# Optimization experiments

Measured on AMD Instinct MI355X. Metric: run time of the kernel, lower is better.

The kernel has to match this reference:

```python
import jax, jax.numpy as jnp
import numpy as np

B, S, D, H, HD, KVH, FF = 2, 2048, 2048, 16, 128, 1, 8192
EPS = 1e-6
ROPE_BASE = 10000.0
NEG = -1e9


def _rms_norm(x, w):
    return x * jax.lax.rsqrt(jnp.mean(x * x, axis=-1, keepdims=True) + EPS) * w


def _rope(t):
    # t: [B, S, H, HD]; standard rotate-half RoPE
    half = HD // 2
    inv_freq = ROPE_BASE ** (-jnp.arange(0, HD, 2, dtype=jnp.float32) / HD)  # [half]
    ang = jnp.arange(S, dtype=jnp.float32)[:, None] * inv_freq               # [S, half]
    cos = jnp.concatenate([jnp.cos(ang), jnp.cos(ang)], axis=-1)[None, :, None, :]
    sin = jnp.concatenate([jnp.sin(ang), jnp.sin(ang)], axis=-1)[None, :, None, :]
    t1, t2 = t[..., :half], t[..., half:]
    rot = jnp.concatenate([-t2, t1], axis=-1)
    return t * cos + rot * sin


def _alibi_bias():
    # slopes for power-of-two head count: 2^(-8*(h+1)/H)
    slopes = 2.0 ** (-8.0 * (jnp.arange(H, dtype=jnp.float32) + 1.0) / H)    # [H]
    pos = jnp.arange(S, dtype=jnp.float32)
    dist = jnp.abs(pos[:, None] - pos[None, :])                              # [S, S]
    return (-slopes[:, None, None] * dist)[None]                             # [1, H, S, S]


def setup_inputs() -> dict:
    key = jax.random.key(0)
    ks = jax.random.split(key, 8)
    sc = lambda fan: 1.0 / np.sqrt(fan)
    x = jax.random.normal(ks[0], (B, S, D), jnp.float32)
    causal = jnp.where(jnp.tril(jnp.ones((S, S), bool)), 0.0, NEG).astype(jnp.float32)[None, None]
    return {
        "x": x,
        "mask": causal,                                                       # [1,1,S,S]
        "w_norm1": jnp.ones((D,), jnp.float32),
        "w_norm2": jnp.ones((D,), jnp.float32),
        "q_w": jax.random.normal(ks[1], (D, D), jnp.float32) * sc(D),        # [out,in] torch layout
        "kv_w": jax.random.normal(ks[2], (KVH * HD * 2, D), jnp.float32) * sc(D),
        "o_w": jax.random.normal(ks[3], (D, D), jnp.float32) * sc(D),
        "w1": jax.random.normal(ks[4], (FF, D), jnp.float32) * sc(D),
        "w2": jax.random.normal(ks[5], (FF, D), jnp.float32) * sc(D),
        "w3": jax.random.normal(ks[6], (D, FF), jnp.float32) * sc(FF),
    }


def reference(x, mask, w_norm1, w_norm2, q_w, kv_w, o_w, w1, w2, w3):
    # --- attention sub-block (pre-norm) ---
    h = _rms_norm(x, w_norm1)
    q = (h @ q_w.T).reshape(B, S, H, HD)                                      # [B,S,H,HD]
    kv = (h @ kv_w.T).reshape(B, S, KVH, 2, HD)
    k = jnp.broadcast_to(kv[:, :, :, 0, :], (B, S, H, HD))                    # MQA expand
    v = jnp.broadcast_to(kv[:, :, :, 1, :], (B, S, H, HD))
    q, k = _rope(q), _rope(k)
    scores = jnp.einsum('bshd,bthd->bhst', q, k) / np.sqrt(HD)                # [B,H,S,S]
    scores = scores + _alibi_bias() + mask
    attn = jax.nn.softmax(scores, axis=-1)
    out = jnp.einsum('bhst,bthd->bshd', attn, v).reshape(B, S, D)
    x = x + out @ o_w.T
    # --- SwiGLU FFN sub-block (pre-norm) ---
    h2 = _rms_norm(x, w_norm2)
    gated = jax.nn.silu(h2 @ w1.T) * (h2 @ w2.T)                              # [B,S,FF]
    return x + gated @ w3.T
```

## Files before the change

kernel.cpp:

```cpp
#include <hip/hip_runtime.h>
#include <stdint.h>

#define NB 2
#define NS 2048
#define ND 2048
#define NH 16
#define NHD 128
#define NFF 8192
#define NBS (NB*NS)
#define NQKV 2304

typedef unsigned short u16;
typedef __attribute__((ext_vector_type(8))) short bf16x8;
typedef __attribute__((ext_vector_type(4))) unsigned short u16x4;
typedef __attribute__((ext_vector_type(4))) float f32x4;

__device__ __forceinline__ u16 f2bf(float f) {
  union { float f; unsigned u; } v; v.f = f;
  unsigned r = v.u + 0x7fffu + ((v.u >> 16) & 1u);
  return (u16)(r >> 16);
}
__device__ __forceinline__ float bf2f(u16 h) {
  union { unsigned u; float f; } v; v.u = ((unsigned)h) << 16;
  return v.f;
}
__device__ __forceinline__ void async_cp16(const void* g, void* l) {
  __builtin_amdgcn_global_load_lds((const __attribute__((address_space(1))) void*)g,
                                   (__attribute__((address_space(3))) void*)l, 16, 0, 0);
}

__global__ void cvt_bf16_kernel(const float* __restrict__ in, u16* __restrict__ out, int n4) {
  int i = blockIdx.x * blockDim.x + threadIdx.x;
  if (i >= n4) return;
  float4 v = reinterpret_cast<const float4*>(in)[i];
  u16x4 o; o.x = f2bf(v.x); o.y = f2bf(v.y); o.z = f2bf(v.z); o.w = f2bf(v.w);
  reinterpret_cast<u16x4*>(out)[i] = o;
}

__global__ __launch_bounds__(256) void rmsnorm_kernel(const float* __restrict__ x,
                                                      const float* __restrict__ w,
                                                      u16* __restrict__ out) {
  const int row = blockIdx.x, tid = threadIdx.x;
  const float* xr = x + (size_t)row * ND;
  float4 a = *reinterpret_cast<const float4*>(xr + tid * 8);
  float4 b = *reinterpret_cast<const float4*>(xr + tid * 8 + 4);
  float ss = a.x*a.x + a.y*a.y + a.z*a.z + a.w*a.w
           + b.x*b.x + b.y*b.y + b.z*b.z + b.w*b.w;
#pragma unroll
  for (int off = 32; off > 0; off >>= 1) ss += __shfl_down(ss, off);
  __shared__ float red[4];
  __shared__ float rinv_s;
  if ((tid & 63) == 0) red[tid >> 6] = ss;
  __syncthreads();
  if (tid == 0) rinv_s = rsqrtf((red[0] + red[1] + red[2] + red[3]) * (1.0f / ND) + 1e-6f);
  __syncthreads();
  const float rinv = rinv_s;
  const float* wr = w + tid * 8;
  u16* orow = out + (size_t)row * ND + tid * 8;
  float vs[8] = {a.x, a.y, a.z, a.w, b.x, b.y, b.z, b.w};
#pragma unroll
  for (int j = 0; j < 8; ++j) orow[j] = f2bf(vs[j] * rinv * wr[j]);
}

__global__ void rope_table_kernel(float* __restrict__ cosT, float* __restrict__ sinT) {
  int i = blockIdx.x * blockDim.x + threadIdx.x;
  if (i >= NS * 64) return;
  int s = i >> 6, d = i & 63;
  float freq = expf(-(float)d * (9.210340371976184f / 64.0f));
  float ang = (float)s * freq;
  cosT[i] = cosf(ang);
  sinT[i] = sinf(ang);
}

__global__ void rope_q_kernel(const u16* __restrict__ qkvraw, const float* __restrict__ cosT,
                              const float* __restrict__ sinT, u16* __restrict__ qout) {
  int i = blockIdx.x * blockDim.x + threadIdx.x;
  if (i >= NB * NS * NH * 64) return;
  int d = i & 63, h = (i >> 6) & 15, s = (i >> 10) & (NS - 1), b = i >> 21;
  size_t rrow = ((size_t)(b * NS + s)) * NQKV + h * NHD;
  float t1 = bf2f(qkvraw[rrow + d]);
  float t2 = bf2f(qkvraw[rrow + d + 64]);
  float c = cosT[(s << 6) + d], sn = sinT[(s << 6) + d];
  const float scale = 0.08838834764831845f;
  size_t orow = (((size_t)(b * NH + h)) * NS + s) * NHD;
  qout[orow + d]      = f2bf((t1 * c - t2 * sn) * scale);
  qout[orow + d + 64] = f2bf((t2 * c + t1 * sn) * scale);
}

__global__ void rope_kv_kernel(const u16* __restrict__ qkvraw, const float* __restrict__ cosT,
                               const float* __restrict__ sinT, u16* __restrict__ kout,
                               u16* __restrict__ vtout) {
  int i = blockIdx.x * blockDim.x + threadIdx.x;
  if (i >= NB * NS * 64) return;
  int d = i & 63, s = (i >> 6) & (NS - 1), b = i >> 17;
  size_t rrow = ((size_t)(b * NS + s)) * NQKV + ND;
  float t1 = bf2f(qkvraw[rrow + d]);
  float t2 = bf2f(qkvraw[rrow + d + 64]);
  float c = cosT[(s << 6) + d], sn = sinT[(s << 6) + d];
  size_t orow = ((size_t)(b * NS + s)) * NHD;
  kout[orow + d]      = f2bf(t1 * c - t2 * sn);
  kout[orow + d + 64] = f2bf(t2 * c + t1 * sn);
  vtout[((size_t)(b * 128 + d)) * NS + s]      = qkvraw[rrow + 128 + d];
  vtout[((size_t)(b * 128 + d + 64)) * NS + s] = qkvraw[rrow + 128 + d + 64];
}

template <int EPI>
__global__ __launch_bounds__(256) void gemm3_kernel(const u16* __restrict__ A,
                                                    const u16* __restrict__ W,
                                                    void* Out, const void* Aux,
                                                    int M, int N, int K) {
  __shared__ __align__(16) char As[128 * 128];
  __shared__ __align__(16) char Bs[128 * 128];
  const int tid = threadIdx.x, wave = tid >> 6, lane = tid & 63;
  const int lm = lane & 15, lg = lane >> 4;

  int bx, by;
  {
    const int gx = gridDim.x;
    if ((gx & 7) == 0) {
      const int id = blockIdx.y * gx + blockIdx.x;
      const int xcd = id & 7, rank = id >> 3;
      const int cw = gx >> 3;
      bx = xcd * cw + rank % cw;
      by = rank / cw;
    } else { bx = blockIdx.x; by = blockIdx.y; }
  }
  const int m0 = by * 128, n0 = bx * 128;
  const int wr = wave >> 1, wc = wave & 1;

  f32x4 acc[4][4];
#pragma unroll
  for (int i = 0; i < 4; ++i)
#pragma unroll
    for (int j = 0; j < 4; ++j) acc[i][j] = (f32x4){0.f, 0.f, 0.f, 0.f};

  for (int k0 = 0; k0 < K; k0 += 64) {
#pragma unroll
    for (int p = 0; p < 4; ++p) {
      int X = p * 4096 + tid * 16;
      int r = X >> 7;
      int sw = ((X >> 4) ^ (X >> 7)) & 7;
      async_cp16(A + (size_t)(m0 + r) * K + k0 + sw * 8, As + p * 4096 + wave * 1024);
      async_cp16(W + (size_t)(n0 + r) * K + k0 + sw * 8, Bs + p * 4096 + wave * 1024);
    }
    __syncthreads();
#pragma unroll
    for (int ks = 0; ks < 2; ++ks) {
      bf16x8 a[4], b[4];
#pragma unroll
      for (int i = 0; i < 4; ++i) {
        const int ra = wr * 64 + i * 16 + lm;
        const int sa = (ks * 4 + lg) ^ (ra & 7);
        a[i] = *(const bf16x8*)(As + ra * 128 + sa * 16);
        const int rb = wc * 64 + i * 16 + lm;
        const int sb = (ks * 4 + lg) ^ (rb & 7);
        b[i] = *(const bf16x8*)(Bs + rb * 128 + sb * 16);
      }
#pragma unroll
      for (int i = 0; i < 4; ++i)
#pragma unroll
        for (int j = 0; j < 4; ++j)
          acc[i][j] = __builtin_amdgcn_mfma_f32_16x16x32_bf16(a[i], b[j], acc[i][j], 0, 0, 0);
    }
    __syncthreads();
  }

#pragma unroll
  for (int i = 0; i < 4; ++i) {
    const int row_b = m0 + wr * 64 + i * 16 + lg * 4;
#pragma unroll
    for (int j = 0; j < 4; ++j) {
      const int col = n0 + wc * 64 + j * 16 + lm;
#pragma unroll
      for (int r = 0; r < 4; ++r) {
        size_t idx = (size_t)(row_b + r) * N + col;
        float v = acc[i][j][r];
        if constexpr (EPI == 0) {
          ((u16*)Out)[idx] = f2bf(v);
        } else if constexpr (EPI == 1) {
          ((float*)Out)[idx] = v + ((const float*)Aux)[idx];
        } else {
          float a1 = bf2f(((const u16*)Aux)[idx]);
          float s = a1 / (1.0f + expf(-a1));
          ((u16*)Out)[idx] = f2bf(s * v);
        }
      }
    }
  }
}

__global__ __launch_bounds__(512) void attn_kernel(const u16* __restrict__ q,
                                                   const u16* __restrict__ kg,
                                                   const u16* __restrict__ vt,
                                                   u16* __restrict__ out) {
  __shared__ __align__(16) u16 Klds[64 * 128];
  __shared__ __align__(16) u16 Vlds[128 * 64];
  __shared__ __align__(16) u16 Plds[8][16 * 72];
  const int tid = threadIdx.x, wave = tid >> 6, lane = tid & 63;
  const int qt = (gridDim.x - 1) - blockIdx.x;
  const int q0 = qt * 128;
  const int bh = blockIdx.y, b = bh >> 4, h = bh & 15;
  const float slope = exp2f(-0.5f * (float)(h + 1));
  const int lm = lane & 15, lg = lane >> 4;
  const int crow = lg * 4;

  bf16x8 qf[4];
  {
    const int qrow = q0 + wave * 16 + lm;
    const u16* qbase = q + ((size_t)bh * NS + qrow) * NHD + lg * 8;
#pragma unroll
    for (int kc = 0; kc < 4; ++kc) qf[kc] = *(const bf16x8*)(qbase + kc * 32);
  }

  float Mr[4], Lr[4];
  f32x4 O[8];
#pragma unroll
  for (int r = 0; r < 4; ++r) { Mr[r] = -__builtin_inff(); Lr[r] = 0.f; }
#pragma unroll
  for (int t = 0; t < 8; ++t) O[t] = (f32x4){0.f, 0.f, 0.f, 0.f};

  u16* pw = Plds[wave];

  const int ntiles = 2 * qt + 2;
  for (int t0 = 0; t0 < ntiles; ++t0) {
    const int kv0 = t0 * 64;
    __syncthreads();
#pragma unroll
    for (int p = 0; p < 2; ++p) {
      int X = p * 8192 + tid * 16;
      int kv = X >> 8;
      int sl = (X >> 4) & 15;
      const u16* src = kg + ((size_t)b * NS + kv0 + kv) * NHD + ((sl ^ (kv & 7)) * 8);
      async_cp16(src, (char*)Klds + p * 8192 + wave * 1024);
    }
#pragma unroll
    for (int p = 0; p < 2; ++p) {
      int X = p * 8192 + tid * 16;
      int d = X >> 7;
      int sl = (X >> 4) & 7;
      const u16* src = vt + ((size_t)b * 128 + d) * NS + kv0 + ((sl ^ (d & 7)) * 8);
      async_cp16(src, (char*)Vlds + p * 8192 + wave * 1024);
    }
    __syncthreads();

    f32x4 sc[4];
#pragma unroll
    for (int sub = 0; sub < 4; ++sub) sc[sub] = (f32x4){0.f, 0.f, 0.f, 0.f};
#pragma unroll
    for (int sub = 0; sub < 4; ++sub) {
      const int kv = sub * 16 + lm;
#pragma unroll
      for (int kc = 0; kc < 4; ++kc) {
        const int slot = (kc * 4 + lg) ^ (kv & 7);
        bf16x8 kf = *(const bf16x8*)((const char*)Klds + kv * 256 + slot * 16);
        sc[sub] = __builtin_amdgcn_mfma_f32_16x16x32_bf16(qf[kc], kf, sc[sub], 0, 0, 0);
      }
    }

    float esc[4], pp[4][4];
#pragma unroll
    for (int r = 0; r < 4; ++r) {
      const int sq = q0 + wave * 16 + crow + r;
      float v[4];
#pragma unroll
      for (int sub = 0; sub < 4; ++sub) {
        const int kc_ = kv0 + sub * 16 + lm;
        v[sub] = (kc_ <= sq) ? sc[sub][r] - slope * (float)(sq - kc_) : -1e9f;
      }
      float mx = fmaxf(fmaxf(v[0], v[1]), fmaxf(v[2], v[3]));
      mx = fmaxf(mx, __shfl_xor(mx, 1));
      mx = fmaxf(mx, __shfl_xor(mx, 2));
      mx = fmaxf(mx, __shfl_xor(mx, 4));
      mx = fmaxf(mx, __shfl_xor(mx, 8));
      const float newM = fmaxf(Mr[r], mx);
      esc[r] = __expf(Mr[r] - newM);
      float rs = 0.f;
#pragma unroll
      for (int sub = 0; sub < 4; ++sub) { pp[sub][r] = __expf(v[sub] - newM); rs += pp[sub][r]; }
      rs += __shfl_xor(rs, 1);
      rs += __shfl_xor(rs, 2);
      rs += __shfl_xor(rs, 4);
      rs += __shfl_xor(rs, 8);
      Lr[r] = Lr[r] * esc[r] + rs;
      Mr[r] = newM;
    }
#pragma unroll
    for (int t = 0; t < 8; ++t) {
      O[t][0] *= esc[0]; O[t][1] *= esc[1]; O[t][2] *= esc[2]; O[t][3] *= esc[3];
    }

#pragma unroll
    for (int sub = 0; sub < 4; ++sub)
#pragma unroll
      for (int r = 0; r < 4; ++r)
        pw[(crow + r) * 72 + sub * 16 + lm] = f2bf(pp[sub][r]);

    bf16x8 pa0 = *(const bf16x8*)&pw[lm * 72 + lg * 8];
    bf16x8 pa1 = *(const bf16x8*)&pw[lm * 72 + 32 + lg * 8];

#pragma unroll
    for (int dt = 0; dt < 8; ++dt) {
      const int d = dt * 16 + lm;
      const int s0 = (lg) ^ (d & 7);
      const int s1 = (4 + lg) ^ (d & 7);
      bf16x8 vf0 = *(const bf16x8*)((const char*)Vlds + d * 128 + s0 * 16);
      bf16x8 vf1 = *(const bf16x8*)((const char*)Vlds + d * 128 + s1 * 16);
      O[dt] = __builtin_amdgcn_mfma_f32_16x16x32_bf16(pa0, vf0, O[dt], 0, 0, 0);
      O[dt] = __builtin_amdgcn_mfma_f32_16x16x32_bf16(pa1, vf1, O[dt], 0, 0, 0);
    }
  }

#pragma unroll
  for (int dt = 0; dt < 8; ++dt) {
#pragma unroll
    for (int r = 0; r < 4; ++r) {
      const int sq = q0 + wave * 16 + crow + r;
      out[((size_t)b * NS + sq) * ND + h * NHD + dt * 16 + lm] = f2bf(O[dt][r] / Lr[r]);
    }
  }
}

extern "C" void kernel_launch(void* const* d_in, const int* in_sizes, int n_in,
                              void* d_out, int out_size, void* d_ws, size_t ws_size,
                              hipStream_t stream) {
  const float* x   = (const float*)d_in[0];
  const float* wn1 = (const float*)d_in[2];
  const float* wn2 = (const float*)d_in[3];
  const float* qw  = (const float*)d_in[4];
  const float* kvw = (const float*)d_in[5];
  const float* ow  = (const float*)d_in[6];
  const float* w1  = (const float*)d_in[7];
  const float* w2  = (const float*)d_in[8];
  const float* w3  = (const float*)d_in[9];
  float* out = (float*)d_out;

  const size_t MiB = 1024 * 1024;
  const size_t NEED = 161 * MiB;
  if (ws_size < NEED) return;

  char* ws = (char*)d_ws;
  u16*   R_W    = (u16*)(ws);
  u16*   QKVRAW = (u16*)(ws + 48 * MiB);
  u16*   AO     = QKVRAW;
  u16*   A1     = (u16*)(ws + 48 * MiB);
  u16*   QB     = (u16*)(ws + 112 * MiB);
  u16*   KB     = (u16*)(ws + 128 * MiB);
  u16*   VT     = (u16*)(ws + 129 * MiB);
  float* X2     = (float*)(ws + 112 * MiB);
  u16*   Hbf    = (u16*)(ws + 144 * MiB);
  float* COS    = (float*)(ws + 160 * MiB);
  float* SIN    = (float*)(ws + 160 * MiB + 512 * 1024);

  auto cvt = [&](const float* src, u16* dst, size_t n) {
    int n4 = (int)(n / 4);
    cvt_bf16_kernel<<<(n4 + 255) / 256, 256, 0, stream>>>(src, dst, n4);
  };

  rope_table_kernel<<<(NS * 64 + 255) / 256, 256, 0, stream>>>(COS, SIN);

  rmsnorm_kernel<<<NBS, 256, 0, stream>>>(x, wn1, Hbf);

  cvt(qw, R_W, (size_t)ND * ND);
  cvt(kvw, R_W + (size_t)ND * ND, (size_t)256 * ND);
  gemm3_kernel<0><<<dim3(NQKV / 128, NBS / 128), 256, 0, stream>>>(
      Hbf, R_W, (void*)QKVRAW, nullptr, NBS, NQKV, ND);

  rope_q_kernel<<<(NB * NS * NH * 64) / 256, 256, 0, stream>>>(QKVRAW, COS, SIN, QB);
  rope_kv_kernel<<<(NB * NS * 64) / 256, 256, 0, stream>>>(QKVRAW, COS, SIN, KB, VT);

  attn_kernel<<<dim3(NS / 128, NB * NH), 512, 0, stream>>>(QB, KB, VT, AO);

  cvt(ow, R_W, (size_t)ND * ND);
  gemm3_kernel<1><<<dim3(ND / 128, NBS / 128), 256, 0, stream>>>(
      AO, R_W, (void*)X2, (const void*)x, NBS, ND, ND);

  rmsnorm_kernel<<<NBS, 256, 0, stream>>>(X2, wn2, Hbf);

  cvt(w1, R_W, (size_t)NFF * ND);
  gemm3_kernel<0><<<dim3(NFF / 128, NBS / 128), 256, 0, stream>>>(
      Hbf, R_W, (void*)A1, nullptr, NBS, NFF, ND);
  cvt(w2, R_W, (size_t)NFF * ND);
  gemm3_kernel<2><<<dim3(NFF / 128, NBS / 128), 256, 0, stream>>>(
      Hbf, R_W, (void*)A1, (const void*)A1, NBS, NFF, ND);

  cvt(w3, R_W, (size_t)ND * NFF);
  gemm3_kernel<1><<<dim3(ND / 128, NBS / 128), 256, 0, stream>>>(
      A1, R_W, (void*)out, (const void*)X2, NBS, ND, NFF);
}
```

Baseline: 875.1 us.

## Fuse SwiGLU gate and up GEMMs into a dual-B kernel; store residual in bf16

Replaces the separate W1 GEMM and the W2 GEMM with a SiLU-multiply epilogue by one kernel. It loads a shared A tile and two weight tiles per K step, keeps two accumulator sets, and writes the gated product once. This removes the bf16 intermediate write and re-read, and the second pass over the activations. The post-attention residual X2 is now stored as bf16 rather than fp32, which shrinks traffic in the RMSNorm and final epilogue but lowers the residual precision. The doubled accumulators raise register pressure and can reduce occupancy.

```diff
diff --git a/kernel.cpp b/kernel.cpp
--- a/kernel.cpp
+++ b/kernel.cpp
@@ -37,15 +37,26 @@
   reinterpret_cast<u16x4*>(out)[i] = o;
 }
 
-__global__ __launch_bounds__(256) void rmsnorm_kernel(const float* __restrict__ x,
+template <int BF16IN>
+__global__ __launch_bounds__(256) void rmsnorm_kernel(const void* __restrict__ xin,
                                                       const float* __restrict__ w,
                                                       u16* __restrict__ out) {
   const int row = blockIdx.x, tid = threadIdx.x;
-  const float* xr = x + (size_t)row * ND;
-  float4 a = *reinterpret_cast<const float4*>(xr + tid * 8);
-  float4 b = *reinterpret_cast<const float4*>(xr + tid * 8 + 4);
-  float ss = a.x*a.x + a.y*a.y + a.z*a.z + a.w*a.w
-           + b.x*b.x + b.y*b.y + b.z*b.z + b.w*b.w;
+  float vs[8];
+  if constexpr (BF16IN == 0) {
+    const float* xr = (const float*)xin + (size_t)row * ND;
+    float4 a = *reinterpret_cast<const float4*>(xr + tid * 8);
+    float4 b = *reinterpret_cast<const float4*>(xr + tid * 8 + 4);
+    vs[0]=a.x; vs[1]=a.y; vs[2]=a.z; vs[3]=a.w; vs[4]=b.x; vs[5]=b.y; vs[6]=b.z; vs[7]=b.w;
+  } else {
+    const u16* xr = (const u16*)xin + (size_t)row * ND;
+    bf16x8 v = *reinterpret_cast<const bf16x8*>(xr + tid * 8);
+#pragma unroll
+    for (int j = 0; j < 8; ++j) vs[j] = bf2f((u16)v[j]);
+  }
+  float ss = 0.f;
+#pragma unroll
+  for (int j = 0; j < 8; ++j) ss += vs[j] * vs[j];
 #pragma unroll
   for (int off = 32; off > 0; off >>= 1) ss += __shfl_down(ss, off);
   __shared__ float red[4];
@@ -57,7 +68,6 @@
   const float rinv = rinv_s;
   const float* wr = w + tid * 8;
   u16* orow = out + (size_t)row * ND + tid * 8;
-  float vs[8] = {a.x, a.y, a.z, a.w, b.x, b.y, b.z, b.w};
 #pragma unroll
   for (int j = 0; j < 8; ++j) orow[j] = f2bf(vs[j] * rinv * wr[j]);
 }
@@ -177,13 +187,97 @@
         float v = acc[i][j][r];
         if constexpr (EPI == 0) {
           ((u16*)Out)[idx] = f2bf(v);
-        } else if constexpr (EPI == 1) {
-          ((float*)Out)[idx] = v + ((const float*)Aux)[idx];
+        } else if constexpr (EPI == 3) {
+          ((u16*)Out)[idx] = f2bf(v + ((const float*)Aux)[idx]);
         } else {
-          float a1 = bf2f(((const u16*)Aux)[idx]);
-          float s = a1 / (1.0f + expf(-a1));
-          ((u16*)Out)[idx] = f2bf(s * v);
+          ((float*)Out)[idx] = v + bf2f(((const u16*)Aux)[idx]);
         }
+      }
+    }
+  }
+}
+
+__global__ __launch_bounds__(256) void gemm3_dual_kernel(const u16* __restrict__ A,
+                                                         const u16* __restrict__ W1,
+                                                         const u16* __restrict__ W2,
+                                                         u16* __restrict__ G,
+                                                         int M, int N, int K) {
+  __shared__ __align__(16) char As[128 * 128];
+  __shared__ __align__(16) char B1s[128 * 128];
+  __shared__ __align__(16) char B2s[128 * 128];
+  const int tid = threadIdx.x, wave = tid >> 6, lane = tid & 63;
+  const int lm = lane & 15, lg = lane >> 4;
+
+  int bx, by;
+  {
+    const int gx = gridDim.x;
+    if ((gx & 7) == 0) {
+      const int id = blockIdx.y * gx + blockIdx.x;
+      const int xcd = id & 7, rank = id >> 3;
+      const int cw = gx >> 3;
+      bx = xcd * cw + rank % cw;
+      by = rank / cw;
+    } else { bx = blockIdx.x; by = blockIdx.y; }
+  }
+  const int m0 = by * 128, n0 = bx * 128;
+  const int wr = wave >> 1, wc = wave & 1;
+
+  f32x4 acc1[4][4], acc2[4][4];
+#pragma unroll
+  for (int i = 0; i < 4; ++i)
+#pragma unroll
+    for (int j = 0; j < 4; ++j) {
+      acc1[i][j] = (f32x4){0.f, 0.f, 0.f, 0.f};
+      acc2[i][j] = (f32x4){0.f, 0.f, 0.f, 0.f};
+    }
+
+  for (int k0 = 0; k0 < K; k0 += 64) {
+#pragma unroll
+    for (int p = 0; p < 4; ++p) {
+      int X = p * 4096 + tid * 16;
+      int r = X >> 7;
+      int sw = ((X >> 4) ^ (X >> 7)) & 7;
+      async_cp16(A  + (size_t)(m0 + r) * K + k0 + sw * 8, As  + p * 4096 + wave * 1024);
+      async_cp16(W1 + (size_t)(n0 + r) * K + k0 + sw * 8, B1s + p * 4096 + wave * 1024);
+      async_cp16(W2 + (size_t)(n0 + r) * K + k0 + sw * 8, B2s + p * 4096 + wave * 1024);
+    }
+    __syncthreads();
+#pragma unroll
+    for (int ks = 0; ks < 2; ++ks) {
+      bf16x8 a[4], b1[4], b2[4];
+#pragma unroll
+      for (int i = 0; i < 4; ++i) {
+        const int ra = wr * 64 + i * 16 + lm;
+        const int sa = (ks * 4 + lg) ^ (ra & 7);
+        a[i] = *(const bf16x8*)(As + ra * 128 + sa * 16);
+        const int rb = wc * 64 + i * 16 + lm;
+        const int sb = (ks * 4 + lg) ^ (rb & 7);
+        b1[i] = *(const bf16x8*)(B1s + rb * 128 + sb * 16);
+        b2[i] = *(const bf16x8*)(B2s + rb * 128 + sb * 16);
+      }
+#pragma unroll
+      for (int i = 0; i < 4; ++i)
+#pragma unroll
+        for (int j = 0; j < 4; ++j) {
+          acc1[i][j] = __builtin_amdgcn_mfma_f32_16x16x32_bf16(a[i], b1[j], acc1[i][j], 0, 0, 0);
+          acc2[i][j] = __builtin_amdgcn_mfma_f32_16x16x32_bf16(a[i], b2[j], acc2[i][j], 0, 0, 0);
+        }
+    }
+    __syncthreads();
+  }
+
+#pragma unroll
+  for (int i = 0; i < 4; ++i) {
+    const int row_b = m0 + wr * 64 + i * 16 + lg * 4;
+#pragma unroll
+    for (int j = 0; j < 4; ++j) {
+      const int col = n0 + wc * 64 + j * 16 + lm;
+#pragma unroll
+      for (int r = 0; r < 4; ++r) {
+        size_t idx = (size_t)(row_b + r) * N + col;
+        float v1 = acc1[i][j][r], v2 = acc2[i][j][r];
+        float s = v1 / (1.0f + expf(-v1));
+        G[idx] = f2bf(s * v2);
       }
     }
   }
@@ -339,14 +433,18 @@
   if (ws_size < NEED) return;
 
   char* ws = (char*)d_ws;
-  u16*   R_W    = (u16*)(ws);
-  u16*   QKVRAW = (u16*)(ws + 48 * MiB);
-  u16*   AO     = QKVRAW;
-  u16*   A1     = (u16*)(ws + 48 * MiB);
+  u16*   WQKV   = (u16*)(ws);
+  u16*   AO     = (u16*)(ws + 16 * MiB);
+  u16*   OWB    = (u16*)(ws + 32 * MiB);
+  u16*   W1B    = (u16*)(ws);
+  u16*   W2B    = (u16*)(ws + 32 * MiB);
+  u16*   W3B    = (u16*)(ws);
+  u16*   QKVRAW = (u16*)(ws + 64 * MiB);
+  u16*   G      = (u16*)(ws + 64 * MiB);
+  u16*   KB     = (u16*)(ws + 83 * MiB);
+  u16*   VT     = (u16*)(ws + 84 * MiB);
   u16*   QB     = (u16*)(ws + 112 * MiB);
-  u16*   KB     = (u16*)(ws + 128 * MiB);
-  u16*   VT     = (u16*)(ws + 129 * MiB);
-  float* X2     = (float*)(ws + 112 * MiB);
+  u16*   X2B    = (u16*)(ws + 128 * MiB);
   u16*   Hbf    = (u16*)(ws + 144 * MiB);
   float* COS    = (float*)(ws + 160 * MiB);
   float* SIN    = (float*)(ws + 160 * MiB + 512 * 1024);
@@ -358,32 +456,30 @@
 
   rope_table_kernel<<<(NS * 64 + 255) / 256, 256, 0, stream>>>(COS, SIN);
 
-  rmsnorm_kernel<<<NBS, 256, 0, stream>>>(x, wn1, Hbf);
-
-  cvt(qw, R_W, (size_t)ND * ND);
-  cvt(kvw, R_W + (size_t)ND * ND, (size_t)256 * ND);
+  rmsnorm_kernel<0><<<NBS, 256, 0, stream>>>(x, wn1, Hbf);
+
+  cvt(qw, WQKV, (size_t)ND * ND);
+  cvt(kvw, WQKV + (size_t)ND * ND, (size_t)256 * ND);
   gemm3_kernel<0><<<dim3(NQKV / 128, NBS / 128), 256, 0, stream>>>(
-      Hbf, R_W, (void*)QKVRAW, nullptr, NBS, NQKV, ND);
+      Hbf, WQKV, (void*)QKVRAW, nullptr, NBS, NQKV, ND);
 
   rope_q_kernel<<<(NB * NS * NH * 64) / 256, 256, 0, stream>>>(QKVRAW, COS, SIN, QB);
   rope_kv_kernel<<<(NB * NS * 64) / 256, 256, 0, stream>>>(QKVRAW, COS, SIN, KB, VT);
 
   attn_kernel<<<dim3(NS / 128, NB * NH), 512, 0, stream>>>(QB, KB, VT, AO);
 
-  cvt(ow, R_W, (size_t)ND * ND);
-  gemm3_kernel<1><<<dim3(ND / 128, NBS / 128), 256, 0, stream>>>(
-      AO, R_W, (void*)X2, (const void*)x, NBS, ND, ND);
-
-  rmsnorm_kernel<<<NBS, 256, 0, stream>>>(X2, wn2, Hbf);
-
-  cvt(w1, R_W, (size_t)NFF * ND);
-  gemm3_kernel<0><<<dim3(NFF / 128, NBS / 128), 256, 0, stream>>>(
-      Hbf, R_W, (void*)A1, nullptr, NBS, NFF, ND);
-  cvt(w2, R_W, (size_t)NFF * ND);
-  gemm3_kernel<2><<<dim3(NFF / 128, NBS / 128), 256, 0, stream>>>(
-      Hbf, R_W, (void*)A1, (const void*)A1, NBS, NFF, ND);
-
-  cvt(w3, R_W, (size_t)ND * NFF);
-  gemm3_kernel<1><<<dim3(ND / 128, NBS / 128), 256, 0, stream>>>(
-      A1, R_W, (void*)out, (const void*)X2, NBS, ND, NFF);
-}
+  cvt(ow, OWB, (size_t)ND * ND);
+  gemm3_kernel<3><<<dim3(ND / 128, NBS / 128), 256, 0, stream>>>(
+      AO, OWB, (void*)X2B, (const void*)x, NBS, ND, ND);
+
+  rmsnorm_kernel<1><<<NBS, 256, 0, stream>>>(X2B, wn2, Hbf);
+
+  cvt(w1, W1B, (size_t)NFF * ND);
+  cvt(w2, W2B, (size_t)NFF * ND);
+  gemm3_dual_kernel<<<dim3(NFF / 128, NBS / 128), 256, 0, stream>>>(
+      Hbf, W1B, W2B, G, NBS, NFF, ND);
+
+  cvt(w3, W3B, (size_t)ND * NFF);
+  gemm3_kernel<4><<<dim3(ND / 128, NBS / 128), 256, 0, stream>>>(
+      G, W3B, (void*)out, (const void*)X2B, NBS, ND, NFF);
+}
```

Measured after the change: 943.3 us. 1.08x slower.
